# Optimization experiments

Measured on AMD Instinct MI355X. Metric: run time of the kernel, lower is better.

Reference implementation:

```python
import jax, jax.numpy as jnp
import numpy as np

D_MODEL = 1024
D_FF = 4 * D_MODEL
NUM_TILES = 8
B, T = 4, 2048


def setup_inputs() -> dict:
    key = jax.random.key(0)
    ks = jax.random.split(key, 7)
    s = 0.02
    return {
        "x": jax.random.normal(ks[0], (B, T, D_MODEL), dtype=jnp.float32),
        "gate_W": jax.random.normal(ks[1], (D_MODEL, NUM_TILES), dtype=jnp.float32) * s,
        "gate_b": jnp.zeros((NUM_TILES,), dtype=jnp.float32),
        "up_W": jax.random.normal(ks[2], (NUM_TILES, D_MODEL, D_FF), dtype=jnp.float32) * s,
        "up_b": jnp.zeros((NUM_TILES, D_FF), dtype=jnp.float32),
        "down_W": jax.random.normal(ks[3], (NUM_TILES, D_FF, D_MODEL), dtype=jnp.float32) * s,
        "down_b": jnp.zeros((NUM_TILES, D_MODEL), dtype=jnp.float32),
    }


def top1_gate(logits):
    # Hard one-hot of argmax; straight-through identity gradient (Top1Gate).
    hard = jax.nn.one_hot(jnp.argmax(logits, axis=-1), logits.shape[-1], dtype=logits.dtype)
    return hard + (logits - jax.lax.stop_gradient(logits))


def trix_linear(x, gate, W, b):
    # x: [N, I], gate: [N, E] one-hot, W: [E, I, O], b: [E, O]
    # Per-tile linear combined by gate weight; loop over small fixed E.
    out = jnp.zeros((x.shape[0], W.shape[2]), dtype=x.dtype)
    for e in range(W.shape[0]):
        out = out + gate[:, e:e + 1] * (x @ W[e] + b[e])
    return out


def reference(x, gate_W, gate_b, up_W, up_b, down_W, down_b):
    Bv, Tv, C = x.shape
    xf = x.reshape(Bv * Tv, C)                      # [N, C]
    gate = top1_gate(xf @ gate_W + gate_b)          # [N, E]
    h = jax.nn.relu(trix_linear(xf, gate, up_W, up_b))   # [N, 4C]
    # dropout in eval mode (identity)
    out = trix_linear(h, gate, down_W, down_b)      # [N, C]
    return out.reshape(Bv, Tv, C), gate.reshape(Bv, Tv, -1)
```

## Files before the change

kernel.cpp:

```cpp
#include <hip/hip_runtime.h>
#include <hip/hip_bf16.h>
#include <stdint.h>

#define NTOK 8192
#define DM   1024
#define DFF  4096
#define NE   8

typedef __bf16 bf16x8 __attribute__((ext_vector_type(8)));
typedef short  short8 __attribute__((ext_vector_type(8)));
typedef float  floatx4 __attribute__((ext_vector_type(4)));

#define WS_CNT   0
#define WS_OFF   64
#define WS_EIDX  1024
#define WS_PERM  (WS_EIDX + NTOK * 4)
#define WS_XPERM (WS_PERM + NTOK * 4)
#define WS_HPERM (WS_XPERM + (size_t)(NTOK + 128) * DM * 2)
#define WS_UPWT  (WS_HPERM + (size_t)(NTOK + 128) * DFF * 2)
#define WS_DWT   (WS_UPWT + (size_t)NE * DM * DFF * 2)

__device__ __forceinline__ unsigned short f2bf(float f) {
  union { float f; unsigned u; } v; v.f = f;
  return (unsigned short)((v.u + 0x7FFFu + ((v.u >> 16) & 1u)) >> 16);
}

__device__ __forceinline__ float f4get(const float4& v, int i) {
  return i == 0 ? v.x : i == 1 ? v.y : i == 2 ? v.z : v.w;
}

__device__ __forceinline__ void gload_lds16(const void* g, void* l) {
  __builtin_amdgcn_global_load_lds(
      (const __attribute__((address_space(1))) unsigned int*)g,
      (__attribute__((address_space(3))) unsigned int*)l, 16, 0, 0);
}

__global__ __launch_bounds__(256) void wconv_kernel(
    const float* __restrict__ W, unsigned short* __restrict__ Wt,
    int K, int N) {
  __shared__ __attribute__((aligned(16))) unsigned short s[64][72];
  int n0 = blockIdx.x * 64;
  int k0 = blockIdx.y * 64;
  const float* Wp = W + (size_t)blockIdx.z * K * N + (size_t)k0 * N + n0;
  int t = threadIdx.x;
  int kr = t >> 4;
  int nc = (t & 15) * 4;
#pragma unroll
  for (int q = 0; q < 4; ++q) {
    float4 v = *(const float4*)(Wp + (size_t)(q * 16 + kr) * N + nc);
    s[nc + 0][q * 16 + kr] = f2bf(v.x);
    s[nc + 1][q * 16 + kr] = f2bf(v.y);
    s[nc + 2][q * 16 + kr] = f2bf(v.z);
    s[nc + 3][q * 16 + kr] = f2bf(v.w);
  }
  __syncthreads();
  int nr = t >> 2;
  int kc = (t & 3) * 16;
  unsigned short* dst = Wt + (size_t)blockIdx.z * N * K + (size_t)(n0 + nr) * K + k0 + kc;
  *(uint4*)dst       = *(const uint4*)&s[nr][kc];
  *(uint4*)(dst + 8) = *(const uint4*)&s[nr][kc + 8];
}

__global__ __launch_bounds__(256) void gate_kernel(
    const float* __restrict__ x, const float* __restrict__ gW,
    const float* __restrict__ gb, float* __restrict__ gate_out,
    int* __restrict__ eidx) {
  int wave = threadIdx.x >> 6;
  int lane = threadIdx.x & 63;
  int t = blockIdx.x * 4 + wave;
  const float4* xr = (const float4*)(x + (size_t)t * DM + lane * 16);
  float acc[8] = {0, 0, 0, 0, 0, 0, 0, 0};
#pragma unroll
  for (int q = 0; q < 4; ++q) {
    float4 xv = xr[q];
    int kbase = lane * 16 + q * 4;
#pragma unroll
    for (int d = 0; d < 4; ++d) {
      float xs = f4get(xv, d);
      const float4* g4 = (const float4*)(gW + (size_t)(kbase + d) * NE);
      float4 g0 = g4[0], g1 = g4[1];
      acc[0] += xs * g0.x; acc[1] += xs * g0.y;
      acc[2] += xs * g0.z; acc[3] += xs * g0.w;
      acc[4] += xs * g1.x; acc[5] += xs * g1.y;
      acc[6] += xs * g1.z; acc[7] += xs * g1.w;
    }
  }
#pragma unroll
  for (int off = 32; off > 0; off >>= 1) {
#pragma unroll
    for (int e = 0; e < 8; ++e) acc[e] += __shfl_down(acc[e], off);
  }
  if (lane == 0) {
    float best = acc[0] + gb[0];
    int bi = 0;
#pragma unroll
    for (int e = 1; e < 8; ++e) {
      float v = acc[e] + gb[e];
      if (v > best) { best = v; bi = e; }
    }
#pragma unroll
    for (int e = 0; e < 8; ++e) gate_out[(size_t)t * NE + e] = (e == bi) ? 1.0f : 0.0f;
    eidx[t] = bi;
  }
}

__global__ __launch_bounds__(1024) void rank_kernel(
    const int* __restrict__ eidx, int* __restrict__ counts,
    int* __restrict__ offs, int* __restrict__ perm) {
  __shared__ unsigned long long sa[1024], sb[1024];
  int tid = threadIdx.x;
  int e8[8];
  unsigned long long ca = 0, cb = 0;
#pragma unroll
  for (int j = 0; j < 8; ++j) {
    int e = eidx[tid * 8 + j];
    e8[j] = e;
    if (e < 4) ca += 1ull << (16 * e);
    else       cb += 1ull << (16 * (e - 4));
  }
  sa[tid] = ca; sb[tid] = cb;
  __syncthreads();
  for (int off = 1; off < 1024; off <<= 1) {
    unsigned long long ta = 0, tb = 0;
    if (tid >= off) { ta = sa[tid - off]; tb = sb[tid - off]; }
    __syncthreads();
    sa[tid] += ta; sb[tid] += tb;
    __syncthreads();
  }
  unsigned long long tot_a = sa[1023], tot_b = sb[1023];
  int cnt_e[8];
#pragma unroll
  for (int e = 0; e < 4; ++e) cnt_e[e] = (int)((tot_a >> (16 * e)) & 0xFFFF);
#pragma unroll
  for (int e = 0; e < 4; ++e) cnt_e[e + 4] = (int)((tot_b >> (16 * e)) & 0xFFFF);
  int off_e[8]; int s = 0;
#pragma unroll
  for (int e = 0; e < 8; ++e) { off_e[e] = s; s += cnt_e[e]; }
  if (tid < 8) { counts[tid] = cnt_e[tid]; offs[tid] = off_e[tid]; }
  unsigned long long ia = sa[tid] - ca, ib = sb[tid] - cb;
  int run[8];
#pragma unroll
  for (int e = 0; e < 4; ++e) run[e] = (int)((ia >> (16 * e)) & 0xFFFF);
#pragma unroll
  for (int e = 0; e < 4; ++e) run[e + 4] = (int)((ib >> (16 * e)) & 0xFFFF);
#pragma unroll
  for (int j = 0; j < 8; ++j) {
    int e = e8[j];
    int pos = off_e[e] + run[e]++;
    perm[pos] = tid * 8 + j;
  }
}

__global__ __launch_bounds__(256) void scatter_data_kernel(
    const float* __restrict__ x, const int* __restrict__ perm,
    unsigned short* __restrict__ xperm) {
  int wave = threadIdx.x >> 6, lane = threadIdx.x & 63;
  int p = blockIdx.x * 4 + wave;
  int t = perm[p];
  const float4* xr = (const float4*)(x + (size_t)t * DM);
#pragma unroll
  for (int q = 0; q < 4; ++q) {
    float4 v = xr[q * 64 + lane];
    uint2 pk;
    pk.x = (unsigned)f2bf(v.x) | ((unsigned)f2bf(v.y) << 16);
    pk.y = (unsigned)f2bf(v.z) | ((unsigned)f2bf(v.w) << 16);
    *(uint2*)(xperm + (size_t)p * DM + q * 256 + lane * 4) = pk;
  }
}

__global__ __launch_bounds__(256) void up_gemm_kernel(
    const unsigned short* __restrict__ xperm,
    const unsigned short* __restrict__ upWt,
    const float* __restrict__ upB,
    const int* __restrict__ counts, const int* __restrict__ offs,
    unsigned short* __restrict__ hperm) {
  const int nwg = NE * 32 * 64;
  int orig = blockIdx.x;
  int wg = (orig & 7) * (nwg >> 3) + (orig >> 3);
  int e  = wg >> 11;
  int r  = wg & 2047;
  int nt = r >> 6;
  int mt = r & 63;
  int cnt = counts[e];
  if (mt * 128 >= cnt) return;
  int row0 = offs[e] + mt * 128;
  int rows_valid = cnt - mt * 128; if (rows_valid > 128) rows_valid = 128;
  int n0 = nt * 128;

  __shared__ __attribute__((aligned(16))) unsigned short sA[128 * 32];
  __shared__ __attribute__((aligned(16))) unsigned short sB[128 * 32];

  int tid = threadIdx.x;
  int wave = tid >> 6, lane = tid & 63;
  int wm = (wave >> 1) * 64, wn = (wave & 1) * 64;

  int srow = wave * 32 + (lane >> 2);
  int scol = (lane & 3) * 8;
  const unsigned short* gA0 = xperm + (size_t)(row0 + srow) * DM + scol;
  const unsigned short* gA1 = gA0 + 16 * DM;
  const unsigned short* gB0 = upWt + (size_t)e * DFF * DM + (size_t)(n0 + srow) * DM + scol;
  const unsigned short* gB1 = gB0 + 16 * DM;
  unsigned short* lA0 = sA + wave * 1024;
  unsigned short* lA1 = lA0 + 512;
  unsigned short* lB0 = sB + wave * 1024;
  unsigned short* lB1 = lB0 + 512;

  floatx4 acc[4][4];
#pragma unroll
  for (int i = 0; i < 4; ++i)
#pragma unroll
    for (int j = 0; j < 4; ++j) acc[i][j] = (floatx4){0.f, 0.f, 0.f, 0.f};

  for (int k0 = 0; k0 < DM; k0 += 32) {
    __syncthreads();
    gload_lds16(gA0 + k0, lA0);
    gload_lds16(gA1 + k0, lA1);
    gload_lds16(gB0 + k0, lB0);
    gload_lds16(gB1 + k0, lB1);
    __syncthreads();
    bf16x8 a[4], b[4];
#pragma unroll
    for (int i = 0; i < 4; ++i)
      a[i] = *(const bf16x8*)(sA + (wm + i * 16 + (lane & 15)) * 32 + (lane >> 4) * 8);
#pragma unroll
    for (int j = 0; j < 4; ++j)
      b[j] = *(const bf16x8*)(sB + (wn + j * 16 + (lane & 15)) * 32 + (lane >> 4) * 8);
#pragma unroll
    for (int i = 0; i < 4; ++i)
#pragma unroll
      for (int j = 0; j < 4; ++j)
        acc[i][j] = __builtin_amdgcn_mfma_f32_16x16x32_bf16(a[i], b[j], acc[i][j], 0, 0, 0);
  }

  const float* ub = upB + (size_t)e * DFF;
#pragma unroll
  for (int i = 0; i < 4; ++i) {
#pragma unroll
    for (int r2 = 0; r2 < 4; ++r2) {
      int rl = wm + i * 16 + (lane >> 4) * 4 + r2;
      if (rl < rows_valid) {
        size_t rowg = (size_t)(row0 + rl) * DFF;
#pragma unroll
        for (int j = 0; j < 4; ++j) {
          int col = n0 + wn + j * 16 + (lane & 15);
          float v = acc[i][j][r2] + ub[col];
          v = v > 0.f ? v : 0.f;
          hperm[rowg + col] = f2bf(v);
        }
      }
    }
  }
}

__global__ __launch_bounds__(256) void down_gemm_kernel(
    const unsigned short* __restrict__ hperm,
    const unsigned short* __restrict__ dWt,
    const float* __restrict__ dB,
    const int* __restrict__ counts, const int* __restrict__ offs,
    const int* __restrict__ perm, float* __restrict__ out) {
  const int nwg = NE * 8 * 64;
  int orig = blockIdx.x;
  int wg = (orig & 7) * (nwg >> 3) + (orig >> 3);
  int e  = wg >> 9;
  int r  = wg & 511;
  int nt = r >> 6;
  int mt = r & 63;
  int cnt = counts[e];
  if (mt * 128 >= cnt) return;
  int row0 = offs[e] + mt * 128;
  int rows_valid = cnt - mt * 128; if (rows_valid > 128) rows_valid = 128;
  int n0 = nt * 128;

  __shared__ __attribute__((aligned(16))) unsigned short sA[128 * 32];
  __shared__ __attribute__((aligned(16))) unsigned short sB[128 * 32];

  int tid = threadIdx.x;
  int wave = tid >> 6, lane = tid & 63;
  int wm = (wave >> 1) * 64, wn = (wave & 1) * 64;

  int srow = wave * 32 + (lane >> 2);
  int scol = (lane & 3) * 8;
  const unsigned short* gA0 = hperm + (size_t)(row0 + srow) * DFF + scol;
  const unsigned short* gA1 = gA0 + 16 * DFF;
  const unsigned short* gB0 = dWt + (size_t)e * DM * DFF + (size_t)(n0 + srow) * DFF + scol;
  const unsigned short* gB1 = gB0 + 16 * DFF;
  unsigned short* lA0 = sA + wave * 1024;
  unsigned short* lA1 = lA0 + 512;
  unsigned short* lB0 = sB + wave * 1024;
  unsigned short* lB1 = lB0 + 512;

  floatx4 acc[4][4];
#pragma unroll
  for (int i = 0; i < 4; ++i)
#pragma unroll
    for (int j = 0; j < 4; ++j) acc[i][j] = (floatx4){0.f, 0.f, 0.f, 0.f};

  for (int k0 = 0; k0 < DFF; k0 += 32) {
    __syncthreads();
    gload_lds16(gA0 + k0, lA0);
    gload_lds16(gA1 + k0, lA1);
    gload_lds16(gB0 + k0, lB0);
    gload_lds16(gB1 + k0, lB1);
    __syncthreads();
    bf16x8 a[4], b[4];
#pragma unroll
    for (int i = 0; i < 4; ++i)
      a[i] = *(const bf16x8*)(sA + (wm + i * 16 + (lane & 15)) * 32 + (lane >> 4) * 8);
#pragma unroll
    for (int j = 0; j < 4; ++j)
      b[j] = *(const bf16x8*)(sB + (wn + j * 16 + (lane & 15)) * 32 + (lane >> 4) * 8);
#pragma unroll
    for (int i = 0; i < 4; ++i)
#pragma unroll
      for (int j = 0; j < 4; ++j)
        acc[i][j] = __builtin_amdgcn_mfma_f32_16x16x32_bf16(a[i], b[j], acc[i][j], 0, 0, 0);
  }

  const float* db = dB + (size_t)e * DM;
#pragma unroll
  for (int i = 0; i < 4; ++i) {
#pragma unroll
    for (int r2 = 0; r2 < 4; ++r2) {
      int rl = wm + i * 16 + (lane >> 4) * 4 + r2;
      if (rl < rows_valid) {
        int token = perm[row0 + rl];
        size_t og = (size_t)token * DM;
#pragma unroll
        for (int j = 0; j < 4; ++j) {
          int col = n0 + wn + j * 16 + (lane & 15);
          out[og + col] = acc[i][j][r2] + db[col];
        }
      }
    }
  }
}

extern "C" void kernel_launch(void* const* d_in, const int* in_sizes, int n_in,
                              void* d_out, int out_size, void* d_ws, size_t ws_size,
                              hipStream_t stream) {
  const float* x   = (const float*)d_in[0];
  const float* gW  = (const float*)d_in[1];
  const float* gb  = (const float*)d_in[2];
  const float* upW = (const float*)d_in[3];
  const float* upB = (const float*)d_in[4];
  const float* dW  = (const float*)d_in[5];
  const float* dB  = (const float*)d_in[6];
  float* out      = (float*)d_out;
  float* gate_out = out + (size_t)NTOK * DM;

  char* ws = (char*)d_ws;
  int* cnt  = (int*)(ws + WS_CNT);
  int* off  = (int*)(ws + WS_OFF);
  int* eidx = (int*)(ws + WS_EIDX);
  int* perm = (int*)(ws + WS_PERM);
  unsigned short* xperm = (unsigned short*)(ws + WS_XPERM);
  unsigned short* hperm = (unsigned short*)(ws + WS_HPERM);
  unsigned short* upWt  = (unsigned short*)(ws + WS_UPWT);
  unsigned short* dWt   = (unsigned short*)(ws + WS_DWT);

  wconv_kernel<<<dim3(DFF / 64, DM / 64, NE), 256, 0, stream>>>(upW, upWt, DM, DFF);
  wconv_kernel<<<dim3(DM / 64, DFF / 64, NE), 256, 0, stream>>>(dW, dWt, DFF, DM);

  gate_kernel<<<NTOK / 4, 256, 0, stream>>>(x, gW, gb, gate_out, eidx);
  rank_kernel<<<1, 1024, 0, stream>>>(eidx, cnt, off, perm);
  scatter_data_kernel<<<NTOK / 4, 256, 0, stream>>>(x, perm, xperm);
  up_gemm_kernel<<<NE * 32 * 64, 256, 0, stream>>>(xperm, upWt, upB, cnt, off, hperm);
  down_gemm_kernel<<<NE * 8 * 64, 256, 0, stream>>>(hperm, dWt, dB, cnt, off, perm, out);
}
```

Before: 626.6 us.

## Double-buffer LDS tiles in up and down expert GEMMs

Both expert GEMM kernels now keep two LDS buffers and issue the global-to-LDS loads for the next K slice before running MFMAs on the current one. This drops one barrier per K step and lets load latency overlap with compute. It doubles LDS use per workgroup, which could lower occupancy. Correctness depends on __syncthreads waiting for the direct-to-LDS loads to complete before the buffer is read.

```diff
diff --git a/kernel.cpp b/kernel.cpp
--- a/kernel.cpp
+++ b/kernel.cpp
@@ -187,8 +187,8 @@
   int rows_valid = cnt - mt * 128; if (rows_valid > 128) rows_valid = 128;
   int n0 = nt * 128;
 
-  __shared__ __attribute__((aligned(16))) unsigned short sA[128 * 32];
-  __shared__ __attribute__((aligned(16))) unsigned short sB[128 * 32];
+  __shared__ __attribute__((aligned(16))) unsigned short sA[2][128 * 32];
+  __shared__ __attribute__((aligned(16))) unsigned short sB[2][128 * 32];
 
   int tid = threadIdx.x;
   int wave = tid >> 6, lane = tid & 63;
@@ -200,10 +200,7 @@
   const unsigned short* gA1 = gA0 + 16 * DM;
   const unsigned short* gB0 = upWt + (size_t)e * DFF * DM + (size_t)(n0 + srow) * DM + scol;
   const unsigned short* gB1 = gB0 + 16 * DM;
-  unsigned short* lA0 = sA + wave * 1024;
-  unsigned short* lA1 = lA0 + 512;
-  unsigned short* lB0 = sB + wave * 1024;
-  unsigned short* lB1 = lB0 + 512;
+  int lofs = wave * 1024;
 
   floatx4 acc[4][4];
 #pragma unroll
@@ -211,26 +208,42 @@
 #pragma unroll
     for (int j = 0; j < 4; ++j) acc[i][j] = (floatx4){0.f, 0.f, 0.f, 0.f};
 
-  for (int k0 = 0; k0 < DM; k0 += 32) {
-    __syncthreads();
-    gload_lds16(gA0 + k0, lA0);
-    gload_lds16(gA1 + k0, lA1);
-    gload_lds16(gB0 + k0, lB0);
-    gload_lds16(gB1 + k0, lB1);
-    __syncthreads();
-    bf16x8 a[4], b[4];
-#pragma unroll
-    for (int i = 0; i < 4; ++i)
-      a[i] = *(const bf16x8*)(sA + (wm + i * 16 + (lane & 15)) * 32 + (lane >> 4) * 8);
-#pragma unroll
-    for (int j = 0; j < 4; ++j)
-      b[j] = *(const bf16x8*)(sB + (wn + j * 16 + (lane & 15)) * 32 + (lane >> 4) * 8);
-#pragma unroll
-    for (int i = 0; i < 4; ++i)
-#pragma unroll
-      for (int j = 0; j < 4; ++j)
-        acc[i][j] = __builtin_amdgcn_mfma_f32_16x16x32_bf16(a[i], b[j], acc[i][j], 0, 0, 0);
-  }
+#define UP_STAGE(P, KK) {                          \
+    gload_lds16(gA0 + (KK), &sA[P][lofs]);         \
+    gload_lds16(gA1 + (KK), &sA[P][lofs + 512]);   \
+    gload_lds16(gB0 + (KK), &sB[P][lofs]);         \
+    gload_lds16(gB1 + (KK), &sB[P][lofs + 512]);   }
+
+#define UP_COMPUTE(P) {                                                          \
+    bf16x8 a[4], b[4];                                                           \
+    _Pragma("unroll")                                                            \
+    for (int i = 0; i < 4; ++i)                                                  \
+      a[i] = *(const bf16x8*)(&sA[P][(wm + i * 16 + (lane & 15)) * 32 + (lane >> 4) * 8]); \
+    _Pragma("unroll")                                                            \
+    for (int j = 0; j < 4; ++j)                                                  \
+      b[j] = *(const bf16x8*)(&sB[P][(wn + j * 16 + (lane & 15)) * 32 + (lane >> 4) * 8]); \
+    _Pragma("unroll")                                                            \
+    for (int i = 0; i < 4; ++i)                                                  \
+      _Pragma("unroll")                                                          \
+      for (int j = 0; j < 4; ++j)                                                \
+        acc[i][j] = __builtin_amdgcn_mfma_f32_16x16x32_bf16(a[i], b[j], acc[i][j], 0, 0, 0); }
+
+  UP_STAGE(0, 0);
+  __syncthreads();
+  for (int k0 = 0; k0 < DM - 64; k0 += 64) {
+    UP_STAGE(1, k0 + 32);
+    UP_COMPUTE(0);
+    __syncthreads();
+    UP_STAGE(0, k0 + 64);
+    UP_COMPUTE(1);
+    __syncthreads();
+  }
+  UP_STAGE(1, DM - 32);
+  UP_COMPUTE(0);
+  __syncthreads();
+  UP_COMPUTE(1);
+#undef UP_STAGE
+#undef UP_COMPUTE
 
   const float* ub = upB + (size_t)e * DFF;
 #pragma unroll
@@ -271,8 +284,8 @@
   int rows_valid = cnt - mt * 128; if (rows_valid > 128) rows_valid = 128;
   int n0 = nt * 128;
 
-  __shared__ __attribute__((aligned(16))) unsigned short sA[128 * 32];
-  __shared__ __attribute__((aligned(16))) unsigned short sB[128 * 32];
+  __shared__ __attribute__((aligned(16))) unsigned short sA[2][128 * 32];
+  __shared__ __attribute__((aligned(16))) unsigned short sB[2][128 * 32];
 
   int tid = threadIdx.x;
   int wave = tid >> 6, lane = tid & 63;
@@ -284,10 +297,7 @@
   const unsigned short* gA1 = gA0 + 16 * DFF;
   const unsigned short* gB0 = dWt + (size_t)e * DM * DFF + (size_t)(n0 + srow) * DFF + scol;
   const unsigned short* gB1 = gB0 + 16 * DFF;
-  unsigned short* lA0 = sA + wave * 1024;
-  unsigned short* lA1 = lA0 + 512;
-  unsigned short* lB0 = sB + wave * 1024;
-  unsigned short* lB1 = lB0 + 512;
+  int lofs = wave * 1024;
 
   floatx4 acc[4][4];
 #pragma unroll
@@ -295,26 +305,42 @@
 #pragma unroll
     for (int j = 0; j < 4; ++j) acc[i][j] = (floatx4){0.f, 0.f, 0.f, 0.f};
 
-  for (int k0 = 0; k0 < DFF; k0 += 32) {
-    __syncthreads();
-    gload_lds16(gA0 + k0, lA0);
-    gload_lds16(gA1 + k0, lA1);
-    gload_lds16(gB0 + k0, lB0);
-    gload_lds16(gB1 + k0, lB1);
-    __syncthreads();
-    bf16x8 a[4], b[4];
-#pragma unroll
-    for (int i = 0; i < 4; ++i)
-      a[i] = *(const bf16x8*)(sA + (wm + i * 16 + (lane & 15)) * 32 + (lane >> 4) * 8);
-#pragma unroll
-    for (int j = 0; j < 4; ++j)
-      b[j] = *(const bf16x8*)(sB + (wn + j * 16 + (lane & 15)) * 32 + (lane >> 4) * 8);
-#pragma unroll
-    for (int i = 0; i < 4; ++i)
-#pragma unroll
-      for (int j = 0; j < 4; ++j)
-        acc[i][j] = __builtin_amdgcn_mfma_f32_16x16x32_bf16(a[i], b[j], acc[i][j], 0, 0, 0);
-  }
+#define DN_STAGE(P, KK) {                          \
+    gload_lds16(gA0 + (KK), &sA[P][lofs]);         \
+    gload_lds16(gA1 + (KK), &sA[P][lofs + 512]);   \
+    gload_lds16(gB0 + (KK), &sB[P][lofs]);         \
+    gload_lds16(gB1 + (KK), &sB[P][lofs + 512]);   }
+
+#define DN_COMPUTE(P) {                                                          \
+    bf16x8 a[4], b[4];                                                           \
+    _Pragma("unroll")                                                            \
+    for (int i = 0; i < 4; ++i)                                                  \
+      a[i] = *(const bf16x8*)(&sA[P][(wm + i * 16 + (lane & 15)) * 32 + (lane >> 4) * 8]); \
+    _Pragma("unroll")                                                            \
+    for (int j = 0; j < 4; ++j)                                                  \
+      b[j] = *(const bf16x8*)(&sB[P][(wn + j * 16 + (lane & 15)) * 32 + (lane >> 4) * 8]); \
+    _Pragma("unroll")                                                            \
+    for (int i = 0; i < 4; ++i)                                                  \
+      _Pragma("unroll")                                                          \
+      for (int j = 0; j < 4; ++j)                                                \
+        acc[i][j] = __builtin_amdgcn_mfma_f32_16x16x32_bf16(a[i], b[j], acc[i][j], 0, 0, 0); }
+
+  DN_STAGE(0, 0);
+  __syncthreads();
+  for (int k0 = 0; k0 < DFF - 64; k0 += 64) {
+    DN_STAGE(1, k0 + 32);
+    DN_COMPUTE(0);
+    __syncthreads();
+    DN_STAGE(0, k0 + 64);
+    DN_COMPUTE(1);
+    __syncthreads();
+  }
+  DN_STAGE(1, DFF - 32);
+  DN_COMPUTE(0);
+  __syncthreads();
+  DN_COMPUTE(1);
+#undef DN_STAGE
+#undef DN_COMPUTE
 
   const float* db = dB + (size_t)e * DM;
 #pragma unroll
```

Result: slower. 644.6 us (+2.9%).

## Triple-buffer grouped GEMMs with 128x256 tiles, 8 waves, and swizzled LDS

Applied to the files above, without the earlier changes.

Both expert GEMMs move from a 128x128 tile with single-buffered K=32 LDS staging to a 128x256 tile with 512 threads, K=64 steps and a three-stage LDS ring. Global-to-LDS loads for step t+2 are issued while step t computes, using explicit vmcnt waits and one barrier per step. An XOR swizzle on the LDS layout is meant to avoid bank conflicts, and s_setprio raises priority around the MFMA bursts. LDS use rises to about 144 KB per block, which limits occupancy to one block per CU, and the grid halves, so tail effects with uneven expert counts may grow.

```diff
diff --git a/kernel.cpp b/kernel.cpp
--- a/kernel.cpp
+++ b/kernel.cpp
@@ -168,42 +168,86 @@
   }
 }
 
-__global__ __launch_bounds__(256) void up_gemm_kernel(
+
+
+#define STG6(pA_, pB_, K0) {                               \
+    gload_lds16(gAs0 + (K0), (pA_) + ldsw);                \
+    gload_lds16(gAs1 + (K0), (pA_) + 4096 + ldsw);         \
+    gload_lds16(gBs0 + (K0), (pB_) + ldsw);                \
+    gload_lds16(gBs1 + (K0), (pB_) + 4096 + ldsw);         \
+    gload_lds16(gBs2 + (K0), (pB_) + 8192 + ldsw);         \
+    gload_lds16(gBs3 + (K0), (pB_) + 12288 + ldsw); }
+
+#define CMP16(pA_, pB_) {                                                        \
+  __builtin_amdgcn_s_setprio(1);                                                 \
+  _Pragma("unroll")                                                              \
+  for (int kk = 0; kk < 2; ++kk) {                                               \
+    int kx = kk ? kx1 : kx0;                                                     \
+    bf16x8 a_[4], b_[4];                                                         \
+    _Pragma("unroll")                                                            \
+    for (int i = 0; i < 4; ++i)                                                  \
+      a_[i] = *(const bf16x8*)((const char*)(pA_) + (wm + i * 16 + l15) * 128 + kx); \
+    _Pragma("unroll")                                                            \
+    for (int j = 0; j < 4; ++j)                                                  \
+      b_[j] = *(const bf16x8*)((const char*)(pB_) + (wn + j * 16 + l15) * 128 + kx); \
+    _Pragma("unroll")                                                            \
+    for (int i = 0; i < 4; ++i)                                                  \
+      _Pragma("unroll")                                                          \
+      for (int j = 0; j < 4; ++j)                                                \
+        acc[i][j] = __builtin_amdgcn_mfma_f32_16x16x32_bf16(a_[i], b_[j], acc[i][j], 0, 0, 0); \
+  }                                                                              \
+  __builtin_amdgcn_s_setprio(0); }
+
+#define VMW(N) asm volatile("s_waitcnt vmcnt(" #N ")" ::: "memory")
+#define BARR { __builtin_amdgcn_s_barrier(); asm volatile("" ::: "memory"); }
+
+__global__ __launch_bounds__(512) void up_gemm_kernel(
     const unsigned short* __restrict__ xperm,
     const unsigned short* __restrict__ upWt,
     const float* __restrict__ upB,
     const int* __restrict__ counts, const int* __restrict__ offs,
     unsigned short* __restrict__ hperm) {
-  const int nwg = NE * 32 * 64;
   int orig = blockIdx.x;
-  int wg = (orig & 7) * (nwg >> 3) + (orig >> 3);
-  int e  = wg >> 11;
-  int r  = wg & 2047;
+  int wg = (orig & 7) * 1024 + (orig >> 3);
+  int e  = wg >> 10;
+  int r  = wg & 1023;
   int nt = r >> 6;
   int mt = r & 63;
   int cnt = counts[e];
   if (mt * 128 >= cnt) return;
   int row0 = offs[e] + mt * 128;
   int rows_valid = cnt - mt * 128; if (rows_valid > 128) rows_valid = 128;
-  int n0 = nt * 128;
-
-  __shared__ __attribute__((aligned(16))) unsigned short sA[128 * 32];
-  __shared__ __attribute__((aligned(16))) unsigned short sB[128 * 32];
+  int n0 = nt * 256;
+
+  __shared__ __attribute__((aligned(16))) unsigned short smem[73728];
+  unsigned short* A_0 = smem;
+  unsigned short* A_1 = smem + 8192;
+  unsigned short* A_2 = smem + 16384;
+  unsigned short* B_0 = smem + 24576;
+  unsigned short* B_1 = smem + 40960;
+  unsigned short* B_2 = smem + 57344;
 
   int tid = threadIdx.x;
-  int wave = tid >> 6, lane = tid & 63;
-  int wm = (wave >> 1) * 64, wn = (wave & 1) * 64;
-
-  int srow = wave * 32 + (lane >> 2);
-  int scol = (lane & 3) * 8;
-  const unsigned short* gA0 = xperm + (size_t)(row0 + srow) * DM + scol;
-  const unsigned short* gA1 = gA0 + 16 * DM;
-  const unsigned short* gB0 = upWt + (size_t)e * DFF * DM + (size_t)(n0 + srow) * DM + scol;
-  const unsigned short* gB1 = gB0 + 16 * DM;
-  unsigned short* lA0 = sA + wave * 1024;
-  unsigned short* lA1 = lA0 + 512;
-  unsigned short* lB0 = sB + wave * 1024;
-  unsigned short* lB1 = lB0 + 512;
+  int wv = tid >> 6, l = tid & 63;
+  int wm = (wv >> 2) * 64;
+  int wn = (wv & 3) * 64;
+  int l15 = l & 15;
+
+  int swz = ((l & 7) ^ (l >> 3)) * 8;
+  int rA  = wv * 8 + (l >> 3);
+  int ldsw = wv * 512;
+  const unsigned short* gAs0 = xperm + (size_t)(row0 + rA) * DM + swz;
+  const unsigned short* gAs1 = gAs0 + (size_t)64 * DM;
+  const unsigned short* Bg   = upWt + (size_t)e * DFF * DM;
+  const unsigned short* gBs0 = Bg + (size_t)(n0 + rA) * DM + swz;
+  const unsigned short* gBs1 = gBs0 + (size_t)64 * DM;
+  const unsigned short* gBs2 = gBs0 + (size_t)128 * DM;
+  const unsigned short* gBs3 = gBs0 + (size_t)192 * DM;
+
+  int hib = (l >> 4) * 16;
+  int swb = (l & 7) << 4;
+  int kx0 = (0  + hib) ^ swb;
+  int kx1 = (64 + hib) ^ swb;
 
   floatx4 acc[4][4];
 #pragma unroll
@@ -211,38 +255,40 @@
 #pragma unroll
     for (int j = 0; j < 4; ++j) acc[i][j] = (floatx4){0.f, 0.f, 0.f, 0.f};
 
-  for (int k0 = 0; k0 < DM; k0 += 32) {
-    __syncthreads();
-    gload_lds16(gA0 + k0, lA0);
-    gload_lds16(gA1 + k0, lA1);
-    gload_lds16(gB0 + k0, lB0);
-    gload_lds16(gB1 + k0, lB1);
-    __syncthreads();
-    bf16x8 a[4], b[4];
-#pragma unroll
-    for (int i = 0; i < 4; ++i)
-      a[i] = *(const bf16x8*)(sA + (wm + i * 16 + (lane & 15)) * 32 + (lane >> 4) * 8);
-#pragma unroll
-    for (int j = 0; j < 4; ++j)
-      b[j] = *(const bf16x8*)(sB + (wn + j * 16 + (lane & 15)) * 32 + (lane >> 4) * 8);
-#pragma unroll
-    for (int i = 0; i < 4; ++i)
-#pragma unroll
-      for (int j = 0; j < 4; ++j)
-        acc[i][j] = __builtin_amdgcn_mfma_f32_16x16x32_bf16(a[i], b[j], acc[i][j], 0, 0, 0);
-  }
+  unsigned short *cA0 = A_0, *cA1 = A_1, *cA2 = A_2;
+  unsigned short *cB0 = B_0, *cB1 = B_1, *cB2 = B_2;
+
+  STG6(cA0, cB0, 0);
+  STG6(cA1, cB1, 64);
+  VMW(6);
+  BARR;
+  const int NT = DM / 64;
+#pragma unroll 1
+  for (int t = 0; t < NT - 2; ++t) {
+    STG6(cA2, cB2, (t + 2) * 64);
+    CMP16(cA0, cB0);
+    VMW(6);
+    BARR;
+    unsigned short* tp;
+    tp = cA0; cA0 = cA1; cA1 = cA2; cA2 = tp;
+    tp = cB0; cB0 = cB1; cB1 = cB2; cB2 = tp;
+  }
+  CMP16(cA0, cB0);
+  VMW(0);
+  BARR;
+  CMP16(cA1, cB1);
 
   const float* ub = upB + (size_t)e * DFF;
 #pragma unroll
   for (int i = 0; i < 4; ++i) {
 #pragma unroll
     for (int r2 = 0; r2 < 4; ++r2) {
-      int rl = wm + i * 16 + (lane >> 4) * 4 + r2;
+      int rl = wm + i * 16 + (l >> 4) * 4 + r2;
       if (rl < rows_valid) {
         size_t rowg = (size_t)(row0 + rl) * DFF;
 #pragma unroll
         for (int j = 0; j < 4; ++j) {
-          int col = n0 + wn + j * 16 + (lane & 15);
+          int col = n0 + wn + j * 16 + l15;
           float v = acc[i][j][r2] + ub[col];
           v = v > 0.f ? v : 0.f;
           hperm[rowg + col] = f2bf(v);
@@ -252,42 +298,53 @@
   }
 }
 
-__global__ __launch_bounds__(256) void down_gemm_kernel(
+__global__ __launch_bounds__(512) void down_gemm_kernel(
     const unsigned short* __restrict__ hperm,
     const unsigned short* __restrict__ dWt,
     const float* __restrict__ dB,
     const int* __restrict__ counts, const int* __restrict__ offs,
     const int* __restrict__ perm, float* __restrict__ out) {
-  const int nwg = NE * 8 * 64;
   int orig = blockIdx.x;
-  int wg = (orig & 7) * (nwg >> 3) + (orig >> 3);
-  int e  = wg >> 9;
-  int r  = wg & 511;
+  int wg = (orig & 7) * 256 + (orig >> 3);
+  int e  = wg >> 8;
+  int r  = wg & 255;
   int nt = r >> 6;
   int mt = r & 63;
   int cnt = counts[e];
   if (mt * 128 >= cnt) return;
   int row0 = offs[e] + mt * 128;
   int rows_valid = cnt - mt * 128; if (rows_valid > 128) rows_valid = 128;
-  int n0 = nt * 128;
-
-  __shared__ __attribute__((aligned(16))) unsigned short sA[128 * 32];
-  __shared__ __attribute__((aligned(16))) unsigned short sB[128 * 32];
+  int n0 = nt * 256;
+
+  __shared__ __attribute__((aligned(16))) unsigned short smem[73728];
+  unsigned short* A_0 = smem;
+  unsigned short* A_1 = smem + 8192;
+  unsigned short* A_2 = smem + 16384;
+  unsigned short* B_0 = smem + 24576;
+  unsigned short* B_1 = smem + 40960;
+  unsigned short* B_2 = smem + 57344;
 
   int tid = threadIdx.x;
-  int wave = tid >> 6, lane = tid & 63;
-  int wm = (wave >> 1) * 64, wn = (wave & 1) * 64;
-
-  int srow = wave * 32 + (lane >> 2);
-  int scol = (lane & 3) * 8;
-  const unsigned short* gA0 = hperm + (size_t)(row0 + srow) * DFF + scol;
-  const unsigned short* gA1 = gA0 + 16 * DFF;
-  const unsigned short* gB0 = dWt + (size_t)e * DM * DFF + (size_t)(n0 + srow) * DFF + scol;
-  const unsigned short* gB1 = gB0 + 16 * DFF;
-  unsigned short* lA0 = sA + wave * 1024;
-  unsigned short* lA1 = lA0 + 512;
-  unsigned short* lB0 = sB + wave * 1024;
-  unsigned short* lB1 = lB0 + 512;
+  int wv = tid >> 6, l = tid & 63;
+  int wm = (wv >> 2) * 64;
+  int wn = (wv & 3) * 64;
+  int l15 = l & 15;
+
+  int swz = ((l & 7) ^ (l >> 3)) * 8;
+  int rA  = wv * 8 + (l >> 3);
+  int ldsw = wv * 512;
+  const unsigned short* gAs0 = hperm + (size_t)(row0 + rA) * DFF + swz;
+  const unsigned short* gAs1 = gAs0 + (size_t)64 * DFF;
+  const unsigned short* Bg   = dWt + (size_t)e * DM * DFF;
+  const unsigned short* gBs0 = Bg + (size_t)(n0 + rA) * DFF + swz;
+  const unsigned short* gBs1 = gBs0 + (size_t)64 * DFF;
+  const unsigned short* gBs2 = gBs0 + (size_t)128 * DFF;
+  const unsigned short* gBs3 = gBs0 + (size_t)192 * DFF;
+
+  int hib = (l >> 4) * 16;
+  int swb = (l & 7) << 4;
+  int kx0 = (0  + hib) ^ swb;
+  int kx1 = (64 + hib) ^ swb;
 
   floatx4 acc[4][4];
 #pragma unroll
@@ -295,39 +352,41 @@
 #pragma unroll
     for (int j = 0; j < 4; ++j) acc[i][j] = (floatx4){0.f, 0.f, 0.f, 0.f};
 
-  for (int k0 = 0; k0 < DFF; k0 += 32) {
-    __syncthreads();
-    gload_lds16(gA0 + k0, lA0);
-    gload_lds16(gA1 + k0, lA1);
-    gload_lds16(gB0 + k0, lB0);
-    gload_lds16(gB1 + k0, lB1);
-    __syncthreads();
-    bf16x8 a[4], b[4];
-#pragma unroll
-    for (int i = 0; i < 4; ++i)
-      a[i] = *(const bf16x8*)(sA + (wm + i * 16 + (lane & 15)) * 32 + (lane >> 4) * 8);
-#pragma unroll
-    for (int j = 0; j < 4; ++j)
-      b[j] = *(const bf16x8*)(sB + (wn + j * 16 + (lane & 15)) * 32 + (lane >> 4) * 8);
-#pragma unroll
-    for (int i = 0; i < 4; ++i)
-#pragma unroll
-      for (int j = 0; j < 4; ++j)
-        acc[i][j] = __builtin_amdgcn_mfma_f32_16x16x32_bf16(a[i], b[j], acc[i][j], 0, 0, 0);
-  }
+  unsigned short *cA0 = A_0, *cA1 = A_1, *cA2 = A_2;
+  unsigned short *cB0 = B_0, *cB1 = B_1, *cB2 = B_2;
+
+  STG6(cA0, cB0, 0);
+  STG6(cA1, cB1, 64);
+  VMW(6);
+  BARR;
+  const int NT = DFF / 64;
+#pragma unroll 1
+  for (int t = 0; t < NT - 2; ++t) {
+    STG6(cA2, cB2, (t + 2) * 64);
+    CMP16(cA0, cB0);
+    VMW(6);
+    BARR;
+    unsigned short* tp;
+    tp = cA0; cA0 = cA1; cA1 = cA2; cA2 = tp;
+    tp = cB0; cB0 = cB1; cB1 = cB2; cB2 = tp;
+  }
+  CMP16(cA0, cB0);
+  VMW(0);
+  BARR;
+  CMP16(cA1, cB1);
 
   const float* db = dB + (size_t)e * DM;
 #pragma unroll
   for (int i = 0; i < 4; ++i) {
 #pragma unroll
     for (int r2 = 0; r2 < 4; ++r2) {
-      int rl = wm + i * 16 + (lane >> 4) * 4 + r2;
+      int rl = wm + i * 16 + (l >> 4) * 4 + r2;
       if (rl < rows_valid) {
         int token = perm[row0 + rl];
         size_t og = (size_t)token * DM;
 #pragma unroll
         for (int j = 0; j < 4; ++j) {
-          int col = n0 + wn + j * 16 + (lane & 15);
+          int col = n0 + wn + j * 16 + l15;
           out[og + col] = acc[i][j][r2] + db[col];
         }
       }
@@ -364,6 +423,6 @@
   gate_kernel<<<NTOK / 4, 256, 0, stream>>>(x, gW, gb, gate_out, eidx);
   rank_kernel<<<1, 1024, 0, stream>>>(eidx, cnt, off, perm);
   scatter_data_kernel<<<NTOK / 4, 256, 0, stream>>>(x, perm, xperm);
-  up_gemm_kernel<<<NE * 32 * 64, 256, 0, stream>>>(xperm, upWt, upB, cnt, off, hperm);
-  down_gemm_kernel<<<NE * 8 * 64, 256, 0, stream>>>(hperm, dWt, dB, cnt, off, perm, out);
-}
+  up_gemm_kernel<<<NE * 16 * 64, 512, 0, stream>>>(xperm, upWt, upB, cnt, off, hperm);
+  down_gemm_kernel<<<NE * 4 * 64, 512, 0, stream>>>(hperm, dWt, dB, cnt, off, perm, out);
+}
```

New measurement: 631.0 us. About the same (+0.7%).
